# Optimization experiments

Hardware: AMD Instinct MI355X
Metric: run time of the kernel (lower is better)

Reference implementation:

```python
import jax, jax.numpy as jnp
import numpy as np

KERNEL_NUM = 20

def _l2norm(x):
    # torch F.normalize: x / max(||x||, eps)
    n = jnp.sqrt(jnp.sum(x * x, axis=-1, keepdims=True))
    return x / jnp.maximum(n, 1e-12)

def setup_inputs() -> dict:
    key = jax.random.key(0)
    ks = jax.random.split(key, 5)
    B, C, H, S, E, V = 32, 5, 50, 20, 300, 60000
    return {
        "candidate_title": jax.random.randint(ks[0], (B, C, S), 0, V),
        "clicked_title": jax.random.randint(ks[1], (B, H, S), 0, V),
        "candidate_title_pad": jnp.ones((B, C, S), jnp.float32),
        "clicked_title_pad": jnp.ones((B, H, S), jnp.float32),
        "embedding": jax.random.normal(ks[2], (V, E), jnp.float32),
        "ltr_w": jax.random.normal(ks[3], (H * KERNEL_NUM, 1), jnp.float32) * 0.03,
        "ltr_b": jax.random.normal(ks[4], (1,), jnp.float32),
    }

def reference(candidate_title, clicked_title, candidate_title_pad, clicked_title_pad, embedding, ltr_w, ltr_b):
    B, C, S = candidate_title.shape
    H = clicked_title.shape[1]
    K = KERNEL_NUM
    dt = embedding.dtype
    mus = (-0.9 + 0.1 * jnp.arange(K, dtype=dt))                    # [K]
    sigmas = jnp.concatenate([jnp.full((K - 1,), 0.1, dt), jnp.full((1,), 0.001, dt)])
    cdd = _l2norm(embedding[candidate_title])                        # [B,C,S,E]
    his = _l2norm(embedding[clicked_title])                          # [B,H,S,E]
    sim = jnp.einsum('bcse,bhte->bchst', cdd, his)                   # [B,C,H,S,S]
    mask_his = clicked_title_pad[:, None, :, None, :, None]          # [B,1,H,1,S,1]
    mask_cdd = candidate_title_pad[:, :, None, :, None]              # [B,C,1,S,1]
    kern = jnp.exp(-((sim[..., None] - mus) ** 2) / (2.0 * sigmas ** 2)) * mask_his  # [B,C,H,S,S,K]
    pooling_sum = jnp.sum(kern, axis=4)                              # [B,C,H,S,K]
    log_pooling = jnp.log(jnp.clip(pooling_sum, 1e-10, None)) * mask_cdd * 0.01
    pooling_vectors = jnp.sum(log_pooling, axis=-2)                  # [B,C,H,K]
    score = pooling_vectors.reshape(B, C, H * K) @ ltr_w + ltr_b     # [B,C,1]
    score = jax.nn.log_softmax(score, axis=1)                        # cdd_size > 1 path
    return jnp.squeeze(score)                                        # [B,C]
```

## Files before the change

### kernel.cpp

```cpp
#include <hip/hip_runtime.h>
#include <hip/hip_fp16.h>

typedef _Float16 half8 __attribute__((ext_vector_type(8)));
typedef float float4v __attribute__((ext_vector_type(4)));

#define E_DIM 300
#define KP 320
#define B_ 32
#define NROW_CDD 3200
#define NROW_HIS 32000
#define NCHUNK 25

__global__ __launch_bounds__(256) void gather_norm(const int* __restrict__ cand,
                                                   const int* __restrict__ clk,
                                                   const float* __restrict__ emb,
                                                   _Float16* __restrict__ outH)
{
    int row  = blockIdx.x * 4 + (threadIdx.x >> 6);
    int lane = threadIdx.x & 63;
    int tok = (row < NROW_CDD) ? cand[row] : clk[row - NROW_CDD];
    const float* e = emb + (long)tok * E_DIM;
    float v[5];
    float ss = 0.f;
#pragma unroll
    for (int j = 0; j < 5; ++j) {
        int idx = lane + j * 64;
        float x = (idx < E_DIM) ? e[idx] : 0.f;
        v[j] = x;
        ss += x * x;
    }
#pragma unroll
    for (int off = 32; off; off >>= 1) ss += __shfl_xor(ss, off);
    float scale = 1.0f / fmaxf(sqrtf(ss), 1e-12f);
    _Float16* o = outH + (long)row * KP;
#pragma unroll
    for (int j = 0; j < 5; ++j) {
        int idx = lane + j * 64;
        o[idx] = (_Float16)((idx < E_DIM) ? v[j] * scale : 0.f);
    }
}

__global__ __launch_bounds__(256) void knrm_fused(const _Float16* __restrict__ wsH,
                                                  const float* __restrict__ cpad,
                                                  const float* __restrict__ hpad,
                                                  const float* __restrict__ ltr_w,
                                                  float* __restrict__ partial)
{
    __shared__ __align__(16) char Bs[40 * 10 * 64 + 512];
    __shared__ _Float16 simH[100 * 42];
    __shared__ float hpS[40];
    __shared__ float wvS[40];
    __shared__ float svals[200];

    int b = blockIdx.y, chunk = blockIdx.x;
    int tid = threadIdx.x;
    int wave = tid >> 6, lane = tid & 63;
    int g = lane >> 4, r16 = lane & 15;

    if (tid < 40) {
        hpS[tid] = hpad[b * 1000 + chunk * 40 + tid];
        wvS[tid] = ltr_w[chunk * 40 + tid];
    }

    const char* gA = (const char*)(wsH + (size_t)b * 100 * KP);
    const char* gB = (const char*)(wsH + (size_t)NROW_CDD * KP + (size_t)b * 1000 * KP);

    for (int u = tid; u < 1600; u += 256) {
        int k = u / 160, rem = u - k * 160;
        int r = rem >> 2, gg = rem & 3;
        int gr = chunk * 40 + r; if (gr > 999) gr = 999;
        *(uint4*)(Bs + (size_t)(k * 40 + r) * 64 + gg * 16) =
            *(const uint4*)(gB + (size_t)gr * 640 + k * 64 + gg * 16);
    }
    __syncthreads();

    float4v acc[2][3];
#pragma unroll
    for (int mi = 0; mi < 2; ++mi)
#pragma unroll
        for (int n = 0; n < 3; ++n) acc[mi][n] = (float4v){0.f, 0.f, 0.f, 0.f};

#pragma unroll 2
    for (int k = 0; k < 10; ++k) {
        half8 bf[3];
#pragma unroll
        for (int n = 0; n < 3; ++n)
            bf[n] = *(const half8*)(Bs + (size_t)(k * 40 + n * 16 + r16) * 64 + g * 16);
#pragma unroll
        for (int mi = 0; mi < 2; ++mi) {
            int m = wave * 2 + mi;
            if (m < 7) {
                int rA = m * 16 + r16; if (rA > 99) rA = 99;
                half8 af = *(const half8*)(gA + (size_t)rA * 640 + k * 64 + g * 16);
#pragma unroll
                for (int n = 0; n < 3; ++n)
                    acc[mi][n] = __builtin_amdgcn_mfma_f32_16x16x32_f16(af, bf[n], acc[mi][n], 0, 0, 0);
            }
        }
    }
#pragma unroll
    for (int mi = 0; mi < 2; ++mi) {
        int m = wave * 2 + mi;
        if (m < 7) {
#pragma unroll
            for (int n = 0; n < 3; ++n) {
                int col = n * 16 + r16;
                if (col < 40) {
#pragma unroll
                    for (int j = 0; j < 4; ++j) {
                        int row = m * 16 + g * 4 + j;
                        if (row < 100) simH[row * 42 + col] = (_Float16)acc[mi][n][j];
                    }
                }
            }
        }
    }
    __syncthreads();

    int unit_h = tid / 100;
    int row = tid - unit_h * 100;

    if (tid < 200) {
        float psum[20];
#pragma unroll
        for (int k = 0; k < 20; ++k) psum[k] = 0.f;

        const _Float16* sp = simH + row * 42 + unit_h * 20;
        const float* mp = hpS + unit_h * 20;
#pragma unroll 4
        for (int t = 0; t < 20; ++t) {
            float s  = (float)sp[t];
            float mm = mp[t];
            float a  = -50.0f * s * s;
#pragma unroll
            for (int k = 0; k < 19; ++k) {
                const float mu = -0.9f + 0.1f * (float)k;
                const float bk = 100.0f * mu;
                const float ck = -50.0f * mu * mu;
                float arg = fmaf(bk, s, a + ck);
                psum[k] = fmaf(__expf(arg), mm, psum[k]);
            }
            float d = s - 1.0f;
            psum[19] = fmaf(__expf(-500000.0f * d * d), mm, psum[19]);
        }
        float val = 0.f;
#pragma unroll
        for (int k = 0; k < 20; ++k)
            val += __logf(fmaxf(psum[k], 1e-10f)) * wvS[unit_h * 20 + k];
        val *= 0.01f * cpad[b * 100 + row];
        svals[row * 2 + unit_h] = val;
    }
    __syncthreads();

    if (tid < 5) {
        float ssum = 0.f;
#pragma unroll
        for (int i = 0; i < 40; ++i) ssum += svals[tid * 40 + i];
        partial[(b * 5 + tid) * NCHUNK + chunk] = ssum;
    }
}

__global__ __launch_bounds__(64) void finalize(const float* __restrict__ partial,
                                               const float* __restrict__ ltr_b,
                                               float* __restrict__ out)
{
    int b = blockIdx.x;
    int tid = threadIdx.x;
    __shared__ float sc[5];
    if (tid < 5) {
        float a = ltr_b[0];
        const float* pp = partial + (b * 5 + tid) * NCHUNK;
#pragma unroll
        for (int ch = 0; ch < NCHUNK; ++ch) a += pp[ch];
        sc[tid] = a;
    }
    __syncthreads();
    if (tid < 5) {
        float m = fmaxf(fmaxf(fmaxf(sc[0], sc[1]), fmaxf(sc[2], sc[3])), sc[4]);
        float sum = 0.f;
#pragma unroll
        for (int i = 0; i < 5; ++i) sum += __expf(sc[i] - m);
        out[b * 5 + tid] = sc[tid] - m - __logf(sum);
    }
}

extern "C" void kernel_launch(void* const* d_in, const int* in_sizes, int n_in,
                              void* d_out, int out_size, void* d_ws, size_t ws_size,
                              hipStream_t stream)
{
    const int*   cand = (const int*)d_in[0];
    const int*   clk  = (const int*)d_in[1];
    const float* cpad = (const float*)d_in[2];
    const float* hpad = (const float*)d_in[3];
    const float* emb  = (const float*)d_in[4];
    const float* lw   = (const float*)d_in[5];
    const float* lb   = (const float*)d_in[6];
    float* out = (float*)d_out;

    _Float16* wsH  = (_Float16*)d_ws;
    float* partial = (float*)((char*)d_ws + (size_t)(NROW_CDD + NROW_HIS) * KP * 2);

    hipLaunchKernelGGL(gather_norm, dim3((NROW_CDD + NROW_HIS) / 4), dim3(256), 0, stream,
                       cand, clk, emb, wsH);
    hipLaunchKernelGGL(knrm_fused, dim3(NCHUNK, B_), dim3(256), 0, stream,
                       wsH, cpad, hpad, lw, partial);
    hipLaunchKernelGGL(finalize, dim3(B_), dim3(64), 0, stream, partial, lb, out);
}
```

Baseline: 53.47 us.

## Stage A and B tiles in LDS via direct global-to-LDS loads with swizzle, larger chunks

The fused KNRM kernel now processes 100 history tokens per block (10 chunks instead of 25) with 512 threads, and loads both the candidate tile and the history tile into LDS using global_load_lds with an XOR swizzle to avoid bank conflicts. Each wave computes a 16x112 similarity strip from LDS, and 500 threads then do the kernel pooling. This cuts redundant global reads of the candidate matrix and the number of blocks. In exchange it uses about 150KB of LDS per block with one block per CU, and gives fewer, larger blocks (320 total).

```diff
diff --git a/kernel.cpp b/kernel.cpp
--- a/kernel.cpp
+++ b/kernel.cpp
@@ -9,7 +9,13 @@
 #define B_ 32
 #define NROW_CDD 3200
 #define NROW_HIS 32000
-#define NCHUNK 25
+#define NCHUNK 10
+
+typedef const void __attribute__((address_space(1))) gvoid;
+typedef void __attribute__((address_space(3))) lvoid;
+__device__ __forceinline__ void gload16(const void* g, void* l) {
+    __builtin_amdgcn_global_load_lds((gvoid*)g, (lvoid*)l, 16, 0, 0);
+}
 
 __global__ __launch_bounds__(256) void gather_norm(const int* __restrict__ cand,
                                                    const int* __restrict__ clk,
@@ -40,93 +46,82 @@
     }
 }
 
-__global__ __launch_bounds__(256) void knrm_fused(const _Float16* __restrict__ wsH,
-                                                  const float* __restrict__ cpad,
-                                                  const float* __restrict__ hpad,
-                                                  const float* __restrict__ ltr_w,
-                                                  float* __restrict__ partial)
-{
-    __shared__ __align__(16) char Bs[40 * 10 * 64 + 512];
-    __shared__ _Float16 simH[100 * 42];
-    __shared__ float hpS[40];
-    __shared__ float wvS[40];
-    __shared__ float svals[200];
+__global__ __launch_bounds__(512, 1) void knrm_fused(const _Float16* __restrict__ wsH,
+                                                     const float* __restrict__ cpad,
+                                                     const float* __restrict__ hpad,
+                                                     const float* __restrict__ ltr_w,
+                                                     float* __restrict__ partial)
+{
+    __shared__ __align__(16) char Abuf[65536];
+    __shared__ __align__(16) char Bbuf[65536];
+    __shared__ _Float16 simL[100 * 102];
+    __shared__ float mS[100];
+    __shared__ float wS[100];
+    __shared__ float cS[100];
+    __shared__ float svals[500];
 
     int b = blockIdx.y, chunk = blockIdx.x;
     int tid = threadIdx.x;
     int wave = tid >> 6, lane = tid & 63;
-    int g = lane >> 4, r16 = lane & 15;
-
-    if (tid < 40) {
-        hpS[tid] = hpad[b * 1000 + chunk * 40 + tid];
-        wvS[tid] = ltr_w[chunk * 40 + tid];
-    }
+    int g4 = lane >> 4, r16 = lane & 15;
 
     const char* gA = (const char*)(wsH + (size_t)b * 100 * KP);
-    const char* gB = (const char*)(wsH + (size_t)NROW_CDD * KP + (size_t)b * 1000 * KP);
-
-    for (int u = tid; u < 1600; u += 256) {
-        int k = u / 160, rem = u - k * 160;
-        int r = rem >> 2, gg = rem & 3;
-        int gr = chunk * 40 + r; if (gr > 999) gr = 999;
-        *(uint4*)(Bs + (size_t)(k * 40 + r) * 64 + gg * 16) =
-            *(const uint4*)(gB + (size_t)gr * 640 + k * 64 + gg * 16);
-    }
-    __syncthreads();
-
-    float4v acc[2][3];
-#pragma unroll
-    for (int mi = 0; mi < 2; ++mi)
-#pragma unroll
-        for (int n = 0; n < 3; ++n) acc[mi][n] = (float4v){0.f, 0.f, 0.f, 0.f};
-
-#pragma unroll 2
-    for (int k = 0; k < 10; ++k) {
-        half8 bf[3];
-#pragma unroll
-        for (int n = 0; n < 3; ++n)
-            bf[n] = *(const half8*)(Bs + (size_t)(k * 40 + n * 16 + r16) * 64 + g * 16);
-#pragma unroll
-        for (int mi = 0; mi < 2; ++mi) {
-            int m = wave * 2 + mi;
-            if (m < 7) {
-                int rA = m * 16 + r16; if (rA > 99) rA = 99;
-                half8 af = *(const half8*)(gA + (size_t)rA * 640 + k * 64 + g * 16);
-#pragma unroll
-                for (int n = 0; n < 3; ++n)
-                    acc[mi][n] = __builtin_amdgcn_mfma_f32_16x16x32_f16(af, bf[n], acc[mi][n], 0, 0, 0);
+    const char* gB = (const char*)(wsH + (size_t)(NROW_CDD + b * 1000 + chunk * 100) * KP);
+
+#pragma unroll
+    for (int c = 0; c < 8; ++c) {
+        int lds_off = wave * 8192 + c * 1024;
+        int my = lds_off + lane * 16;
+        int r = my / 640;
+        int src = my ^ ((r & 7) << 4);
+        gload16(gA + src, Abuf + lds_off);
+        gload16(gB + src, Bbuf + lds_off);
+    }
+    if (tid < 100) {
+        mS[tid] = hpad[b * 1000 + chunk * 100 + tid];
+        wS[tid] = ltr_w[chunk * 100 + tid];
+        cS[tid] = cpad[b * 100 + tid];
+    }
+    __syncthreads();
+
+    if (wave < 7) {
+        float4v acc[7];
+#pragma unroll
+        for (int n = 0; n < 7; ++n) acc[n] = (float4v){0.f, 0.f, 0.f, 0.f};
+        int rA = wave * 16 + r16; if (rA > 99) rA = 99;
+#pragma unroll
+        for (int k = 0; k < 10; ++k) {
+            half8 af = *(const half8*)(Abuf + ((rA * 640 + k * 64 + g4 * 16) ^ ((rA & 7) << 4)));
+#pragma unroll
+            for (int n = 0; n < 7; ++n) {
+                int rB = n * 16 + r16; if (rB > 99) rB = 99;
+                half8 bf = *(const half8*)(Bbuf + ((rB * 640 + k * 64 + g4 * 16) ^ ((rB & 7) << 4)));
+                acc[n] = __builtin_amdgcn_mfma_f32_16x16x32_f16(af, bf, acc[n], 0, 0, 0);
             }
         }
-    }
-#pragma unroll
-    for (int mi = 0; mi < 2; ++mi) {
-        int m = wave * 2 + mi;
-        if (m < 7) {
-#pragma unroll
-            for (int n = 0; n < 3; ++n) {
-                int col = n * 16 + r16;
-                if (col < 40) {
-#pragma unroll
-                    for (int j = 0; j < 4; ++j) {
-                        int row = m * 16 + g * 4 + j;
-                        if (row < 100) simH[row * 42 + col] = (_Float16)acc[mi][n][j];
-                    }
+#pragma unroll
+        for (int n = 0; n < 7; ++n) {
+            int col = n * 16 + r16;
+            if (col < 100) {
+#pragma unroll
+                for (int j = 0; j < 4; ++j) {
+                    int rr = wave * 16 + g4 * 4 + j;
+                    if (rr < 100) simL[rr * 102 + col] = (_Float16)acc[n][j];
                 }
             }
         }
     }
     __syncthreads();
 
-    int unit_h = tid / 100;
-    int row = tid - unit_h * 100;
-
-    if (tid < 200) {
+    if (tid < 500) {
+        int h = tid / 100;
+        int row = tid - h * 100;
         float psum[20];
 #pragma unroll
         for (int k = 0; k < 20; ++k) psum[k] = 0.f;
 
-        const _Float16* sp = simH + row * 42 + unit_h * 20;
-        const float* mp = hpS + unit_h * 20;
+        const _Float16* sp = simL + row * 102 + h * 20;
+        const float* mp = mS + h * 20;
 #pragma unroll 4
         for (int t = 0; t < 20; ++t) {
             float s  = (float)sp[t];
@@ -135,27 +130,27 @@
 #pragma unroll
             for (int k = 0; k < 19; ++k) {
                 const float mu = -0.9f + 0.1f * (float)k;
-                const float bk = 100.0f * mu;
-                const float ck = -50.0f * mu * mu;
-                float arg = fmaf(bk, s, a + ck);
+                float arg = fmaf(100.0f * mu, s, a - 50.0f * mu * mu);
                 psum[k] = fmaf(__expf(arg), mm, psum[k]);
             }
             float d = s - 1.0f;
             psum[19] = fmaf(__expf(-500000.0f * d * d), mm, psum[19]);
         }
         float val = 0.f;
+        const float* wp = wS + h * 20;
 #pragma unroll
         for (int k = 0; k < 20; ++k)
-            val += __logf(fmaxf(psum[k], 1e-10f)) * wvS[unit_h * 20 + k];
-        val *= 0.01f * cpad[b * 100 + row];
-        svals[row * 2 + unit_h] = val;
+            val += __logf(fmaxf(psum[k], 1e-10f)) * wp[k];
+        svals[tid] = val * 0.01f * cS[row];
     }
     __syncthreads();
 
     if (tid < 5) {
         float ssum = 0.f;
-#pragma unroll
-        for (int i = 0; i < 40; ++i) ssum += svals[tid * 40 + i];
+        for (int h = 0; h < 5; ++h)
+#pragma unroll
+            for (int r = 0; r < 20; ++r)
+                ssum += svals[h * 100 + tid * 20 + r];
         partial[(b * 5 + tid) * NCHUNK + chunk] = ssum;
     }
 }
@@ -198,11 +193,11 @@
     float* out = (float*)d_out;
 
     _Float16* wsH  = (_Float16*)d_ws;
-    float* partial = (float*)((char*)d_ws + (size_t)(NROW_CDD + NROW_HIS) * KP * 2);
+    float* partial = (float*)((char*)d_ws + (size_t)(NROW_CDD + NROW_HIS) * KP * 2 + 4096);
 
     hipLaunchKernelGGL(gather_norm, dim3((NROW_CDD + NROW_HIS) / 4), dim3(256), 0, stream,
                        cand, clk, emb, wsH);
-    hipLaunchKernelGGL(knrm_fused, dim3(NCHUNK, B_), dim3(256), 0, stream,
+    hipLaunchKernelGGL(knrm_fused, dim3(NCHUNK, B_), dim3(512), 0, stream,
                        wsH, cpad, hpad, lw, partial);
     hipLaunchKernelGGL(finalize, dim3(B_), dim3(64), 0, stream, partial, lb, out);
 }
```

Result: no change. 52.77 us (-1.3%).

## Use 7 waves per block with register-resident A tiles and swizzled B staging

Applied to the files above, without the earlier changes.

Changes the knrm_fused block from 4 to 7 waves, so each wave owns one 16-row M tile. Each wave preloads its entire A fragment (all 10 k-steps) into registers up front instead of reloading from global inside the k loop. B is staged into shared memory in a row-contiguous layout with an XOR swizzle to avoid bank conflicts, and cpad is cached in shared memory. This trades higher register use and a larger block for more MFMA parallelism and fewer serialized global loads, while the exp-heavy pooling phase still uses only 200 threads.

```diff
diff --git a/kernel.cpp b/kernel.cpp
--- a/kernel.cpp
+++ b/kernel.cpp
@@ -40,93 +40,90 @@
     }
 }
 
-__global__ __launch_bounds__(256) void knrm_fused(const _Float16* __restrict__ wsH,
-                                                  const float* __restrict__ cpad,
-                                                  const float* __restrict__ hpad,
-                                                  const float* __restrict__ ltr_w,
-                                                  float* __restrict__ partial)
-{
-    __shared__ __align__(16) char Bs[40 * 10 * 64 + 512];
-    __shared__ _Float16 simH[100 * 42];
+__global__ __launch_bounds__(448, 2) void knrm_fused(const _Float16* __restrict__ wsH,
+                                                     const float* __restrict__ cpad,
+                                                     const float* __restrict__ hpad,
+                                                     const float* __restrict__ ltr_w,
+                                                     float* __restrict__ partial)
+{
+    __shared__ __align__(16) char Bbuf[40 * 640 + 128];
+    __shared__ _Float16 simT[100 * 42];
     __shared__ float hpS[40];
     __shared__ float wvS[40];
+    __shared__ float cS[100];
     __shared__ float svals[200];
 
     int b = blockIdx.y, chunk = blockIdx.x;
     int tid = threadIdx.x;
     int wave = tid >> 6, lane = tid & 63;
-    int g = lane >> 4, r16 = lane & 15;
-
+    int g4 = lane >> 4, r16 = lane & 15;
+
+    const char* gA = (const char*)(wsH + (size_t)b * 100 * KP);
+    const char* gB = (const char*)(wsH + (size_t)(NROW_CDD + b * 1000 + chunk * 40) * KP);
+
+    int rA = wave * 16 + r16; if (rA > 99) rA = 99;
+    const char* pA = gA + (size_t)rA * 640;
+    half8 af[10];
+#pragma unroll
+    for (int k = 0; k < 10; ++k) af[k] = *(const half8*)(pA + k * 64 + g4 * 16);
+
+    uint4 bv[4];
+#pragma unroll
+    for (int j = 0; j < 4; ++j) {
+        int u = tid + 448 * j; if (u > 1599) u = 1599;
+        bv[j] = *(const uint4*)(gB + (size_t)u * 16);
+    }
+#pragma unroll
+    for (int j = 0; j < 4; ++j) {
+        int u = tid + 448 * j;
+        if (u < 1600) {
+            int r = u / 40;
+            *(uint4*)(Bbuf + ((u * 16) ^ ((r & 7) << 4))) = bv[j];
+        }
+    }
     if (tid < 40) {
         hpS[tid] = hpad[b * 1000 + chunk * 40 + tid];
         wvS[tid] = ltr_w[chunk * 40 + tid];
     }
-
-    const char* gA = (const char*)(wsH + (size_t)b * 100 * KP);
-    const char* gB = (const char*)(wsH + (size_t)NROW_CDD * KP + (size_t)b * 1000 * KP);
-
-    for (int u = tid; u < 1600; u += 256) {
-        int k = u / 160, rem = u - k * 160;
-        int r = rem >> 2, gg = rem & 3;
-        int gr = chunk * 40 + r; if (gr > 999) gr = 999;
-        *(uint4*)(Bs + (size_t)(k * 40 + r) * 64 + gg * 16) =
-            *(const uint4*)(gB + (size_t)gr * 640 + k * 64 + gg * 16);
-    }
-    __syncthreads();
-
-    float4v acc[2][3];
-#pragma unroll
-    for (int mi = 0; mi < 2; ++mi)
-#pragma unroll
-        for (int n = 0; n < 3; ++n) acc[mi][n] = (float4v){0.f, 0.f, 0.f, 0.f};
-
-#pragma unroll 2
+    if (tid >= 64 && tid < 164) cS[tid - 64] = cpad[b * 100 + (tid - 64)];
+    __syncthreads();
+
+    float4v acc[3];
+#pragma unroll
+    for (int n = 0; n < 3; ++n) acc[n] = (float4v){0.f, 0.f, 0.f, 0.f};
+
+#pragma unroll
     for (int k = 0; k < 10; ++k) {
-        half8 bf[3];
-#pragma unroll
-        for (int n = 0; n < 3; ++n)
-            bf[n] = *(const half8*)(Bs + (size_t)(k * 40 + n * 16 + r16) * 64 + g * 16);
-#pragma unroll
-        for (int mi = 0; mi < 2; ++mi) {
-            int m = wave * 2 + mi;
-            if (m < 7) {
-                int rA = m * 16 + r16; if (rA > 99) rA = 99;
-                half8 af = *(const half8*)(gA + (size_t)rA * 640 + k * 64 + g * 16);
-#pragma unroll
-                for (int n = 0; n < 3; ++n)
-                    acc[mi][n] = __builtin_amdgcn_mfma_f32_16x16x32_f16(af, bf[n], acc[mi][n], 0, 0, 0);
+#pragma unroll
+        for (int n = 0; n < 3; ++n) {
+            int rB = n * 16 + r16; if (rB > 39) rB = 39;
+            half8 bf = *(const half8*)(Bbuf + ((rB * 640 + k * 64 + g4 * 16) ^ ((rB & 7) << 4)));
+            acc[n] = __builtin_amdgcn_mfma_f32_16x16x32_f16(af[k], bf, acc[n], 0, 0, 0);
+        }
+    }
+
+#pragma unroll
+    for (int n = 0; n < 3; ++n) {
+        int col = n * 16 + r16;
+        if (col < 40) {
+#pragma unroll
+            for (int j = 0; j < 4; ++j) {
+                int r = wave * 16 + g4 * 4 + j;
+                if (r < 100) simT[r * 42 + col] = (_Float16)acc[n][j];
             }
         }
     }
-#pragma unroll
-    for (int mi = 0; mi < 2; ++mi) {
-        int m = wave * 2 + mi;
-        if (m < 7) {
-#pragma unroll
-            for (int n = 0; n < 3; ++n) {
-                int col = n * 16 + r16;
-                if (col < 40) {
-#pragma unroll
-                    for (int j = 0; j < 4; ++j) {
-                        int row = m * 16 + g * 4 + j;
-                        if (row < 100) simH[row * 42 + col] = (_Float16)acc[mi][n][j];
-                    }
-                }
-            }
-        }
-    }
-    __syncthreads();
-
-    int unit_h = tid / 100;
-    int row = tid - unit_h * 100;
+    __syncthreads();
 
     if (tid < 200) {
+        int hl = tid / 100;
+        int row = tid - hl * 100;
         float psum[20];
 #pragma unroll
         for (int k = 0; k < 20; ++k) psum[k] = 0.f;
 
-        const _Float16* sp = simH + row * 42 + unit_h * 20;
-        const float* mp = hpS + unit_h * 20;
+        const _Float16* sp = simT + row * 42 + hl * 20;
+        const float* mp = hpS + hl * 20;
 #pragma unroll 4
         for (int t = 0; t < 20; ++t) {
             float s  = (float)sp[t];
@@ -135,20 +132,18 @@
 #pragma unroll
             for (int k = 0; k < 19; ++k) {
                 const float mu = -0.9f + 0.1f * (float)k;
-                const float bk = 100.0f * mu;
-                const float ck = -50.0f * mu * mu;
-                float arg = fmaf(bk, s, a + ck);
+                float arg = fmaf(100.0f * mu, s, a - 50.0f * mu * mu);
                 psum[k] = fmaf(__expf(arg), mm, psum[k]);
             }
             float d = s - 1.0f;
             psum[19] = fmaf(__expf(-500000.0f * d * d), mm, psum[19]);
         }
         float val = 0.f;
+        const float* wp = wvS + hl * 20;
 #pragma unroll
         for (int k = 0; k < 20; ++k)
-            val += __logf(fmaxf(psum[k], 1e-10f)) * wvS[unit_h * 20 + k];
-        val *= 0.01f * cpad[b * 100 + row];
-        svals[row * 2 + unit_h] = val;
+            val += __logf(fmaxf(psum[k], 1e-10f)) * wp[k];
+        svals[row * 2 + hl] = val * 0.01f * cS[row];
     }
     __syncthreads();
 
@@ -202,7 +197,7 @@
 
     hipLaunchKernelGGL(gather_norm, dim3((NROW_CDD + NROW_HIS) / 4), dim3(256), 0, stream,
                        cand, clk, emb, wsH);
-    hipLaunchKernelGGL(knrm_fused, dim3(NCHUNK, B_), dim3(256), 0, stream,
+    hipLaunchKernelGGL(knrm_fused, dim3(NCHUNK, B_), dim3(448), 0, stream,
                        wsH, cpad, hpad, lw, partial);
     hipLaunchKernelGGL(finalize, dim3(B_), dim3(64), 0, stream, partial, lb, out);
 }
```

Result: faster. 46.82 us (-12.4%).
